# Performance work log

Hardware: AMD Instinct MI355X
Metric: run time of the kernel (lower is better)

The kernel has to match this reference:

```python
import jax, jax.numpy as jnp
import numpy as np

NODES = 81
NODE_DIM = 2
IN_DIM = NODES * NODE_DIM  # 162
D = 256
H = 16
HD = D // H
DFF = 2048
T, B, E = 1024, 8, 648


def _layernorm(x, w, b, eps=1e-5):
    m = x.mean(-1, keepdims=True)
    v = x.var(-1, keepdims=True)
    return (x - m) / jnp.sqrt(v + eps) * w + b


def setup_inputs() -> dict:
    key = jax.random.key(0)
    ks = jax.random.split(key, 12)
    s = 0.02
    W = lambda k, shape: jax.random.normal(k, shape, jnp.float32) * s
    return {
        "src": jax.random.normal(ks[0], (T, B, IN_DIM), jnp.float32),
        "edge_index": jax.random.randint(ks[1], (2, E), 0, NODES),
        "gcn_w": W(ks[2], (NODE_DIM, NODE_DIM)),
        "gcn_b": jnp.zeros((NODE_DIM,), jnp.float32),
        "fc_w": W(ks[3], (IN_DIM, D)),
        "fc_b": jnp.zeros((D,), jnp.float32),
        "wq": W(ks[4], (D, D)), "bq": jnp.zeros((D,), jnp.float32),
        "wk": W(ks[5], (D, D)), "bk": jnp.zeros((D,), jnp.float32),
        "wv": W(ks[6], (D, D)), "bv": jnp.zeros((D,), jnp.float32),
        "wo": W(ks[7], (D, D)), "bo": jnp.zeros((D,), jnp.float32),
        "ln1_w": jnp.ones((D,), jnp.float32), "ln1_b": jnp.zeros((D,), jnp.float32),
        "ffn_w1": W(ks[8], (D, DFF)), "ffn_b1": jnp.zeros((DFF,), jnp.float32),
        "ffn_w2": W(ks[9], (DFF, D)), "ffn_b2": jnp.zeros((D,), jnp.float32),
        "ln2_w": jnp.ones((D,), jnp.float32), "ln2_b": jnp.zeros((D,), jnp.float32),
        "dec_w": W(ks[10], (D, IN_DIM)), "dec_b": jnp.zeros((IN_DIM,), jnp.float32),
    }


def reference(src, edge_index, gcn_w, gcn_b, fc_w, fc_b, wq, bq, wk, bk, wv, bv,
              wo, bo, ln1_w, ln1_b, ffn_w1, ffn_b1, ffn_w2, ffn_b2, ln2_w, ln2_b,
              dec_w, dec_b):
    t, b, _ = src.shape
    # ---- batched GCNConv(2,2): all T*B tiny graphs share one adjacency ----
    # src[t,b] = [in_flow(81), out_flow(81)] -> node features [81, 2]
    xg = jnp.swapaxes(src.reshape(t, b, NODE_DIM, NODES), -1, -2)  # [T,B,81,2]
    row, col = edge_index[0], edge_index[1]
    A = jnp.zeros((NODES, NODES), src.dtype).at[col, row].add(1.0)
    A = A + jnp.eye(NODES, dtype=src.dtype)          # add self-loops
    deg = A.sum(1)
    dinv = jnp.where(deg > 0, 1.0 / jnp.sqrt(deg), 0.0)
    A_hat = dinv[:, None] * A * dinv[None, :]        # D^-1/2 (A+I) D^-1/2
    hg = jnp.einsum('ij,tbjc->tbic', A_hat, xg @ gcn_w) + gcn_b  # [T,B,81,2]
    # gcn_output.transpose(0,1).view(-1): channel-major flatten
    src2 = jnp.swapaxes(hg, -1, -2).reshape(t, b, IN_DIM)
    # ---- fc + positional encoding ----
    x = src2 @ fc_w + fc_b  # [T,B,D]
    pos = jnp.arange(t, dtype=jnp.float32)[:, None]
    div = jnp.exp(jnp.arange(0, D, 2, dtype=jnp.float32) * (-np.log(10000.0) / D))
    pe = jnp.zeros((t, D), x.dtype).at[:, 0::2].set(jnp.sin(pos * div))
    pe = pe.at[:, 1::2].set(jnp.cos(pos * div))
    x = x + pe[:, None, :]
    # ---- TransformerEncoderLayer (post-norm, relu, causal mask, eval) ----
    q = (x @ wq + bq).reshape(t, b, H, HD)
    k = (x @ wk + bk).reshape(t, b, H, HD)
    v = (x @ wv + bv).reshape(t, b, H, HD)
    scores = jnp.einsum('tbhd,sbhd->bhts', q, k) / jnp.sqrt(jnp.asarray(HD, x.dtype))
    causal = jnp.tril(jnp.ones((t, t), bool))
    scores = jnp.where(causal, scores, jnp.finfo(x.dtype).min)
    attn = jax.nn.softmax(scores, axis=-1)
    ctx = jnp.einsum('bhts,sbhd->tbhd', attn, v).reshape(t, b, D) @ wo + bo
    x = _layernorm(x + ctx, ln1_w, ln1_b)
    ff = jax.nn.relu(x @ ffn_w1 + ffn_b1) @ ffn_w2 + ffn_b2
    x = _layernorm(x + ff, ln2_w, ln2_b)
    return x @ dec_w + dec_b  # [T,B,162]
```

## Files before the change

### kernel.cpp

```cpp
#include <hip/hip_runtime.h>
#include <math.h>

#define T_    1024
#define B_    8
#define D_    256
#define H_    16
#define HD_   16
#define DFF_  2048
#define NODES_ 81
#define INDIM_ 162
#define E_    648
#define M_    (T_*B_)

typedef __bf16 bf16x8 __attribute__((ext_vector_type(8)));
typedef float  f32x4  __attribute__((ext_vector_type(4)));
typedef unsigned short ushort_t;
typedef unsigned int   uint_t;

union bfpack { bf16x8 v; uint_t u[4]; };

__device__ __forceinline__ ushort_t f2bf(float f) {
    union { float f; uint_t u; } c; c.f = f;
    uint_t u = c.u;
    uint_t r = u + 0x7fffu + ((u >> 16) & 1u);
    return (ushort_t)(r >> 16);
}

__device__ __forceinline__ uint_t fbits(float f) {
    union { float f; uint_t u; } c; c.f = f;
    return c.u;
}

__device__ __forceinline__ bf16x8 zero8() {
    bf16x8 v;
#pragma unroll
    for (int e = 0; e < 8; e++) v[e] = (__bf16)0.0f;
    return v;
}

__device__ __forceinline__ void gload_lds16(const void* g, void* l) {
    __builtin_amdgcn_global_load_lds(
        (const __attribute__((address_space(1))) void*)g,
        (__attribute__((address_space(3))) void*)l, 16, 0, 0);
}

__device__ __forceinline__ void trans_tile(
        const float* __restrict__ in, ushort_t* __restrict__ out,
        float (*tile)[33], int K, int N, int Kp, int bx, int by) {
    int k0 = bx * 32, n0 = by * 32;
    int tx = threadIdx.x & 31, ty = threadIdx.x >> 5;
#pragma unroll
    for (int i = 0; i < 4; i++) {
        int r = k0 + ty + i * 8, c = n0 + tx;
        tile[ty + i * 8][tx] = (r < K && c < N) ? in[(size_t)r * N + c] : 0.f;
    }
    __syncthreads();
#pragma unroll
    for (int i = 0; i < 4; i++) {
        int r = n0 + ty + i * 8, c = k0 + tx;
        out[(size_t)r * Kp + c] = f2bf(tile[tx][ty + i * 8]);
    }
}

__global__ __launch_bounds__(256) void prep_all(
        const int* __restrict__ edge, const float* __restrict__ gcn_w,
        const float* __restrict__ gcn_b, const float* __restrict__ fc_w,
        const float* __restrict__ fc_b, const float* __restrict__ src,
        const float* __restrict__ wq, const float* __restrict__ wk,
        const float* __restrict__ wv, const float* __restrict__ wo,
        const float* __restrict__ dec_w, const float* __restrict__ w1,
        const float* __restrict__ w2,
        const float* __restrict__ bq, const float* __restrict__ bk,
        const float* __restrict__ bv,
        ushort_t* __restrict__ weffT, float* __restrict__ beff,
        ushort_t* __restrict__ srcb,
        ushort_t* __restrict__ wqkvT, ushort_t* __restrict__ woT,
        ushort_t* __restrict__ dwT, ushort_t* __restrict__ w1T,
        ushort_t* __restrict__ w2T, float* __restrict__ qkvbias) {
    __shared__ float A[NODES_ * NODES_];
    __shared__ float dinv[NODES_];
    __shared__ float tile[32][33];
    int bid = blockIdx.x;
    int tid = threadIdx.x;
    if (bid < 82) {
        for (int i = tid; i < NODES_ * NODES_; i += 256) A[i] = 0.f;
        __syncthreads();
        for (int e = tid; e < E_; e += 256) {
            int r = edge[e];
            int c = edge[E_ + e];
            atomicAdd(&A[c * NODES_ + r], 1.0f);
        }
        __syncthreads();
        if (tid < NODES_) A[tid * NODES_ + tid] += 1.0f;
        __syncthreads();
        if (tid < NODES_) {
            float s = 0.f;
            for (int k = 0; k < NODES_; k++) s += A[tid * NODES_ + k];
            dinv[tid] = (s > 0.f) ? rsqrtf(s) : 0.f;
        }
        __syncthreads();
        int d = tid, j = bid;
        if (j < NODES_) {
            float s0 = 0.f, s1 = 0.f;
            for (int i = 0; i < NODES_; i++) {
                float a = dinv[i] * A[i * NODES_ + j] * dinv[j];
                s0 += a * fc_w[(0 * NODES_ + i) * D_ + d];
                s1 += a * fc_w[(1 * NODES_ + i) * D_ + d];
            }
            weffT[d * 192 + j]          = f2bf(gcn_w[0] * s0 + gcn_w[1] * s1);
            weffT[d * 192 + NODES_ + j] = f2bf(gcn_w[2] * s0 + gcn_w[3] * s1);
        } else {
            float t0 = 0.f, t1 = 0.f;
            for (int i = 0; i < NODES_; i++) {
                t0 += fc_w[(0 * NODES_ + i) * D_ + d];
                t1 += fc_w[(1 * NODES_ + i) * D_ + d];
            }
            beff[d] = fc_b[d] + gcn_b[0] * t0 + gcn_b[1] * t1;
            for (int c = INDIM_; c < 192; c++) weffT[d * 192 + c] = 0;
        }
    } else if (bid < 1426) {
        int l = bid - 82;
        if (l < 64)        trans_tile(wq,    wqkvT,          tile, D_,   D_,     D_,   l & 7,  l >> 3);
        else if (l < 128)  trans_tile(wk,    wqkvT + 65536,  tile, D_,   D_,     D_,   (l-64) & 7,  (l-64) >> 3);
        else if (l < 192)  trans_tile(wv,    wqkvT + 131072, tile, D_,   D_,     D_,   (l-128) & 7, (l-128) >> 3);
        else if (l < 256)  trans_tile(wo,    woT,            tile, D_,   D_,     D_,   (l-192) & 7, (l-192) >> 3);
        else if (l < 320)  trans_tile(dec_w, dwT,            tile, D_,   INDIM_, D_,   (l-256) & 7, (l-256) >> 3);
        else if (l < 832)  trans_tile(w1,    w1T,            tile, D_,   DFF_,   D_,   (l-320) & 7, (l-320) >> 3);
        else               trans_tile(w2,    w2T,            tile, DFF_, D_,     DFF_, (l-832) & 63, (l-832) >> 6);
    } else if (bid == 1426) {
#pragma unroll
        for (int k = 0; k < 3; k++) {
            int i = k * 256 + tid;
            qkvbias[i] = (i < 256) ? bq[i] : ((i < 512) ? bk[i - 256] : bv[i - 512]);
        }
    } else {
        int blk = bid - 1427;
        size_t row0 = (size_t)blk * 64;
        const float* sp = src + row0 * INDIM_;
        ushort_t* dp = srcb + row0 * 192;
        for (int i = tid; i < 64 * INDIM_; i += 256) {
            int r = i / INDIM_;
            int c = i - r * INDIM_;
            dp[(size_t)r * 192 + c] = f2bf(sp[i]);
        }
        for (int i = tid; i < 64 * 30; i += 256) {
            int r = i / 30;
            int c = i - r * 30;
            dp[(size_t)r * 192 + INDIM_ + c] = 0;
        }
    }
}

enum { EP_PE = 0, EP_QKV = 1, EP_PLAIN = 2, EP_RELU = 3, EP_DEC = 4, EP_PART = 5 };

template <int EPI, int TM, int KS>
__global__ __launch_bounds__(256) void gemm_bf16(
        const ushort_t* __restrict__ A, const ushort_t* __restrict__ BT,
        const float* __restrict__ bias, float* __restrict__ Cf,
        ushort_t* __restrict__ Cb, int M, int N, int K) {
    __shared__ ushort_t sA[TM * 64];
    __shared__ ushort_t sB[128 * 64];
    int tid = threadIdx.x;
    int w = tid >> 6, lane = tid & 63;
    int cc = lane & 15, q = lane >> 4;
    int bm = blockIdx.y * TM, bn = blockIdx.x * 128;
    int part = (KS > 1) ? blockIdx.z : 0;
    int kbeg = part * (K / KS), kend = kbeg + K / KS;

    int srow = (lane >> 3);
    int sslot = lane & 7;

    const int NJ = (TM == 128) ? 4 : 2;
    int mbase = (TM == 128) ? ((w >> 1) * 64) : 0;
    int nbase = (TM == 128) ? ((w & 1) * 64) : (w * 32);

    f32x4 acc[4][NJ];
#pragma unroll
    for (int i = 0; i < 4; i++)
#pragma unroll
        for (int j = 0; j < NJ; j++)
#pragma unroll
            for (int e = 0; e < 4; e++) acc[i][j][e] = 0.f;

    for (int k0 = kbeg; k0 < kend; k0 += 64) {
        if (TM == 128) {
#pragma unroll
            for (int i = 0; i < 4; i++) {
                int r = w * 32 + i * 8 + srow;
                const ushort_t* ga = A + (size_t)(bm + r) * K + k0 + ((sslot ^ (r & 7)) * 8);
                gload_lds16(ga, &sA[(w * 32 + i * 8) * 64]);
            }
        } else {
#pragma unroll
            for (int i = 0; i < 2; i++) {
                int r = w * 16 + i * 8 + srow;
                const ushort_t* ga = A + (size_t)(bm + r) * K + k0 + ((sslot ^ (r & 7)) * 8);
                gload_lds16(ga, &sA[(w * 16 + i * 8) * 64]);
            }
        }
#pragma unroll
        for (int i = 0; i < 4; i++) {
            int r = w * 32 + i * 8 + srow;
            const ushort_t* gb = BT + (size_t)(bn + r) * K + k0 + ((sslot ^ (r & 7)) * 8);
            gload_lds16(gb, &sB[(w * 32 + i * 8) * 64]);
        }
        __syncthreads();
#pragma unroll
        for (int ks = 0; ks < 2; ks++) {
            bf16x8 af[4], bfr[NJ];
#pragma unroll
            for (int i = 0; i < 4; i++) {
                int m = mbase + i * 16 + cc;
                int off = m * 64 + (((ks * 4 + q) ^ (cc & 7)) * 8);
                af[i] = *(const bf16x8*)&sA[off];
            }
#pragma unroll
            for (int j = 0; j < NJ; j++) {
                int n = nbase + j * 16 + cc;
                int off = n * 64 + (((ks * 4 + q) ^ (cc & 7)) * 8);
                bfr[j] = *(const bf16x8*)&sB[off];
            }
#pragma unroll
            for (int i = 0; i < 4; i++)
#pragma unroll
                for (int j = 0; j < NJ; j++)
                    acc[i][j] = __builtin_amdgcn_mfma_f32_16x16x32_bf16(af[i], bfr[j], acc[i][j], 0, 0, 0);
        }
        __syncthreads();
    }

#pragma unroll
    for (int i = 0; i < 4; i++) {
#pragma unroll
        for (int j = 0; j < NJ; j++) {
            int col = bn + nbase + j * 16 + cc;
            float bv = 0.f;
            if (EPI == EP_DEC) bv = (col < INDIM_) ? bias[col] : 0.f;
            else if (EPI != EP_PART) bv = bias[col];
#pragma unroll
            for (int reg = 0; reg < 4; reg++) {
                int row = bm + mbase + i * 16 + q * 4 + reg;
                float v = acc[i][j][reg] + bv;
                if (EPI == EP_PE) {
                    int t = row >> 3;
                    float freq = __expf((float)(col & ~1) * (-9.210340371976184f / 256.f));
                    float ang = (float)t * freq;
                    v += (col & 1) ? __cosf(ang) : __sinf(ang);
                    Cf[(size_t)row * N + col] = v;
                    Cb[(size_t)row * N + col] = f2bf(v);
                } else if (EPI == EP_QKV) {
                    int t = row >> 3, b = row & 7;
                    int nn = col & 255, which = col >> 8;
                    int h = nn >> 4, hd = nn & 15;
                    float vq = (which == 0) ? v * 0.25f : v;
                    Cb[(size_t)which * 2097152 +
                       ((size_t)((b * H_ + h) * T_ + t)) * HD_ + hd] = f2bf(vq);
                } else if (EPI == EP_PLAIN) {
                    Cf[(size_t)row * N + col] = v;
                } else if (EPI == EP_RELU) {
                    v = fmaxf(v, 0.f);
                    Cb[(size_t)row * N + col] = f2bf(v);
                } else if (EPI == EP_DEC) {
                    if (col < INDIM_) Cf[(size_t)row * INDIM_ + col] = v;
                } else if (EPI == EP_PART) {
                    Cf[(size_t)part * M * N + (size_t)row * N + col] = v;
                }
            }
        }
    }
}

__global__ __launch_bounds__(256) void attn_mfma(
        const ushort_t* __restrict__ Qb, const ushort_t* __restrict__ Kb,
        const ushort_t* __restrict__ Vb, float* __restrict__ partO,
        float* __restrict__ partL) {
    const int qc_of[20] = {0,1,2,2,3,3,4,4,4,5,5,5,6,6,6,6,7,7,7,7};
    const int kp_of[20] = {0,0,0,1,0,1,0,1,2,0,1,2,0,1,2,3,0,1,2,3};
    int slot = blockIdx.x;
    int qc = qc_of[slot], kp = kp_of[slot];
    int bh = blockIdx.y;
    int tid = threadIdx.x;
    int w = tid >> 6, lane = tid & 63;
    int cc = lane & 15, q = lane >> 4;
    int qb0 = qc * 128;
    int kbeg = kp * 4;
    int kend = 2 * (qc + 1);
    if (kend > kbeg + 4) kend = kbeg + 4;

    __shared__ ushort_t VTs[2][16 * 72];

    const ushort_t* Qp = Qb + (size_t)bh * (T_ * HD_);
    const ushort_t* Kp = Kb + (size_t)bh * (T_ * HD_);
    const ushort_t* Vp = Vb + (size_t)bh * (T_ * HD_);

    bf16x8 qf[2];
#pragma unroll
    for (int i = 0; i < 2; i++) {
        if (q < 2)
            qf[i] = *(const bf16x8*)&Qp[(size_t)(qb0 + w * 32 + i * 16 + cc) * HD_ + q * 8];
        else
            qf[i] = zero8();
    }

    f32x4 ot[2];
    float lsum[2];
#pragma unroll
    for (int i = 0; i < 2; i++) {
        lsum[i] = 0.f;
#pragma unroll
        for (int e = 0; e < 4; e++) ot[i][e] = 0.f;
    }

    int qmaxw = qb0 + w * 32 + 31;

    for (int kb = kbeg; kb < kend; kb++) {
        ushort_t* vbuf = VTs[kb & 1];
        {
            int r = tid >> 2, c0 = (tid & 3) * 4;
            ushort4 vv = *(const ushort4*)&Vp[(size_t)(kb * 64 + r) * HD_ + c0];
            vbuf[(c0 + 0) * 72 + r] = vv.x;
            vbuf[(c0 + 1) * 72 + r] = vv.y;
            vbuf[(c0 + 2) * 72 + r] = vv.z;
            vbuf[(c0 + 3) * 72 + r] = vv.w;
        }
        __syncthreads();
        if (kb * 64 > qmaxw) continue;

        bf16x8 kf[4];
#pragma unroll
        for (int j = 0; j < 4; j++) {
            if (q < 2)
                kf[j] = *(const bf16x8*)&Kp[(size_t)(kb * 64 + j * 16 + cc) * HD_ + q * 8];
            else
                kf[j] = zero8();
        }

        f32x4 s[2][4];
#pragma unroll
        for (int j = 0; j < 4; j++)
#pragma unroll
            for (int i = 0; i < 2; i++) {
                f32x4 z;
#pragma unroll
                for (int e = 0; e < 4; e++) z[e] = 0.f;
                s[i][j] = __builtin_amdgcn_mfma_f32_16x16x32_bf16(kf[j], qf[i], z, 0, 0, 0);
            }

#pragma unroll
        for (int jj = 0; jj < 2; jj++) {
            int j0 = jj * 2, j1 = j0 + 1;
            bfpack af;
            const uint_t* vt0 = (const uint_t*)&vbuf[cc * 72 + j0 * 16 + q * 4];
            const uint_t* vt1 = (const uint_t*)&vbuf[cc * 72 + j1 * 16 + q * 4];
            af.u[0] = vt0[0]; af.u[1] = vt0[1];
            af.u[2] = vt1[0]; af.u[3] = vt1[1];
            int key00 = kb * 64 + j0 * 16 + q * 4;
            int key01 = key00 + 16;
#pragma unroll
            for (int i = 0; i < 2; i++) {
                float p0 = __expf(s[i][j0][0]);
                float p1 = __expf(s[i][j0][1]);
                float p2 = __expf(s[i][j0][2]);
                float p3 = __expf(s[i][j0][3]);
                float p4 = __expf(s[i][j1][0]);
                float p5 = __expf(s[i][j1][1]);
                float p6 = __expf(s[i][j1][2]);
                float p7 = __expf(s[i][j1][3]);
                int qsub = qb0 + w * 32 + i * 16;
                if (kb * 64 + j0 * 16 + 15 > qsub) {
                    int qrow = qsub + cc;
                    if (key00 + 0 > qrow) p0 = 0.f;
                    if (key00 + 1 > qrow) p1 = 0.f;
                    if (key00 + 2 > qrow) p2 = 0.f;
                    if (key00 + 3 > qrow) p3 = 0.f;
                }
                if (kb * 64 + j1 * 16 + 15 > qsub) {
                    int qrow = qsub + cc;
                    if (key01 + 0 > qrow) p4 = 0.f;
                    if (key01 + 1 > qrow) p5 = 0.f;
                    if (key01 + 2 > qrow) p6 = 0.f;
                    if (key01 + 3 > qrow) p7 = 0.f;
                }
                bfpack pf;
                pf.u[0] = (fbits(p0) >> 16) | (fbits(p1) & 0xffff0000u);
                pf.u[1] = (fbits(p2) >> 16) | (fbits(p3) & 0xffff0000u);
                pf.u[2] = (fbits(p4) >> 16) | (fbits(p5) & 0xffff0000u);
                pf.u[3] = (fbits(p6) >> 16) | (fbits(p7) & 0xffff0000u);
                ot[i] = __builtin_amdgcn_mfma_f32_16x16x32_bf16(af.v, pf.v, ot[i], 0, 0, 0);
                lsum[i] += ((p0 + p1) + (p2 + p3)) + ((p4 + p5) + (p6 + p7));
            }
        }
    }

    int base = (bh * 20 + slot) * 128;
#pragma unroll
    for (int i = 0; i < 2; i++) {
        float l = lsum[i];
        l += __shfl_xor(l, 16);
        l += __shfl_xor(l, 32);
        int row = w * 32 + i * 16 + cc;
        *(f32x4*)&partO[((size_t)(base + row)) * 16 + q * 4] = ot[i];
        if (q == 0) partL[base + row] = l;
    }
}

__global__ __launch_bounds__(256) void attn_reduce(
        const float* __restrict__ partO, const float* __restrict__ partL,
        ushort_t* __restrict__ ctxb) {
    const int cum[9] = {0, 1, 2, 4, 6, 9, 12, 16, 20};
    int qc = blockIdx.x, bh = blockIdx.y;
    int row = threadIdx.x >> 1, dh = threadIdx.x & 1;
    int p0 = cum[qc], p1 = cum[qc + 1];
    float o[8];
#pragma unroll
    for (int e = 0; e < 8; e++) o[e] = 0.f;
    float l = 0.f;
    for (int p = p0; p < p1; p++) {
        size_t base = ((size_t)bh * 20 + p) * 128 + row;
        const float4 a = *(const float4*)&partO[base * 16 + dh * 8];
        const float4 b4 = *(const float4*)&partO[base * 16 + dh * 8 + 4];
        o[0] += a.x; o[1] += a.y; o[2] += a.z; o[3] += a.w;
        o[4] += b4.x; o[5] += b4.y; o[6] += b4.z; o[7] += b4.w;
        l += partL[base];
    }
    float inv = 1.f / l;
    int t = qc * 128 + row, b = bh >> 4, h = bh & 15;
    ushort_t* op = ctxb + ((size_t)t * B_ + b) * D_ + h * HD_ + dh * 8;
    ushort4 u0, u1;
    u0.x = f2bf(o[0] * inv); u0.y = f2bf(o[1] * inv);
    u0.z = f2bf(o[2] * inv); u0.w = f2bf(o[3] * inv);
    u1.x = f2bf(o[4] * inv); u1.y = f2bf(o[5] * inv);
    u1.z = f2bf(o[6] * inv); u1.w = f2bf(o[7] * inv);
    *(ushort4*)&op[0] = u0;
    *(ushort4*)&op[4] = u1;
}

template <int NP, bool HASB>
__global__ __launch_bounds__(256) void ln_kernel(
        const float* __restrict__ X, const float* __restrict__ P0,
        const float* __restrict__ P1, const float* __restrict__ RB,
        const float* __restrict__ w, const float* __restrict__ b,
        float* __restrict__ out, ushort_t* __restrict__ outb) {
    int wv = threadIdx.x >> 6, lane = threadIdx.x & 63;
    int row = blockIdx.x * 4 + wv;
    int c = lane * 4;
    const float4 x4 = *(const float4*)&X[(size_t)row * D_ + c];
    const float4 p4 = *(const float4*)&P0[(size_t)row * D_ + c];
    float v0 = x4.x + p4.x, v1 = x4.y + p4.y, v2 = x4.z + p4.z, v3 = x4.w + p4.w;
    if (NP == 2) {
        const float4 q4 = *(const float4*)&P1[(size_t)row * D_ + c];
        v0 += q4.x; v1 += q4.y; v2 += q4.z; v3 += q4.w;
    }
    if (HASB) {
        const float4 r4 = *(const float4*)&RB[c];
        v0 += r4.x; v1 += r4.y; v2 += r4.z; v3 += r4.w;
    }
    float s  = v0 + v1 + v2 + v3;
    float sq = v0 * v0 + v1 * v1 + v2 * v2 + v3 * v3;
    for (int off = 32; off; off >>= 1) {
        s  += __shfl_xor(s, off);
        sq += __shfl_xor(sq, off);
    }
    float mean = s * (1.f / 256.f);
    float var  = sq * (1.f / 256.f) - mean * mean;
    float rstd = rsqrtf(var + 1e-5f);
    float o0 = (v0 - mean) * rstd * w[c + 0] + b[c + 0];
    float o1 = (v1 - mean) * rstd * w[c + 1] + b[c + 1];
    float o2 = (v2 - mean) * rstd * w[c + 2] + b[c + 2];
    float o3 = (v3 - mean) * rstd * w[c + 3] + b[c + 3];
    float4 o; o.x = o0; o.y = o1; o.z = o2; o.w = o3;
    *(float4*)&out[(size_t)row * D_ + c] = o;
    ushort4 ob;
    ob.x = f2bf(o0); ob.y = f2bf(o1); ob.z = f2bf(o2); ob.w = f2bf(o3);
    *(ushort4*)&outb[(size_t)row * D_ + c] = ob;
}

extern "C" void kernel_launch(void* const* d_in, const int* in_sizes, int n_in,
                              void* d_out, int out_size, void* d_ws, size_t ws_size,
                              hipStream_t stream) {
    (void)in_sizes; (void)n_in; (void)out_size; (void)ws_size;
    const float* src     = (const float*)d_in[0];
    const int*   edge    = (const int*)d_in[1];
    const float* gcn_w   = (const float*)d_in[2];
    const float* gcn_b   = (const float*)d_in[3];
    const float* fc_w    = (const float*)d_in[4];
    const float* fc_b    = (const float*)d_in[5];
    const float* wq      = (const float*)d_in[6];
    const float* bq      = (const float*)d_in[7];
    const float* wk      = (const float*)d_in[8];
    const float* bk      = (const float*)d_in[9];
    const float* wv      = (const float*)d_in[10];
    const float* bv      = (const float*)d_in[11];
    const float* wo      = (const float*)d_in[12];
    const float* bo      = (const float*)d_in[13];
    const float* ln1_w   = (const float*)d_in[14];
    const float* ln1_b   = (const float*)d_in[15];
    const float* ffn_w1  = (const float*)d_in[16];
    const float* ffn_b1  = (const float*)d_in[17];
    const float* ffn_w2  = (const float*)d_in[18];
    const float* ffn_b2  = (const float*)d_in[19];
    const float* ln2_w   = (const float*)d_in[20];
    const float* ln2_b   = (const float*)d_in[21];
    const float* dec_w   = (const float*)d_in[22];
    const float* dec_b   = (const float*)d_in[23];
    float* out = (float*)d_out;

    float* ws = (float*)d_ws;
    float* beff    = ws;
    float* qkvbias = ws + 256;
    float* x0      = ws + 1024;
    float* tmp     = x0  + 2097152;
    float* tmp2    = tmp + 2097152;
    float* x1      = tmp2 + 2097152;
    float* x2s     = x1  + 2097152;
    ushort_t* ub   = (ushort_t*)(ws + 10486784);
    ushort_t* srcb = ub;
    ushort_t* x0b  = ub + 1572864;
    ushort_t* x1b  = x0b + 2097152;
    ushort_t* x2b  = x1b + 2097152;
    ushort_t* ctxb = x2b + 2097152;
    ushort_t* hb   = ctxb + 2097152;
    ushort_t* qkvb = hb + 16777216;
    ushort_t* weffT= qkvb + 6291456;
    ushort_t* wqkvT= weffT + 49152;
    ushort_t* woT  = wqkvT + 196608;
    ushort_t* w1T  = woT + 65536;
    ushort_t* w2T  = w1T + 524288;
    ushort_t* dwT  = w2T + 524288;
    float* partO = (float*)hb;
    float* partL = partO + 5242880;

    prep_all<<<1555, 256, 0, stream>>>(edge, gcn_w, gcn_b, fc_w, fc_b, src,
                                       wq, wk, wv, wo, dec_w, ffn_w1, ffn_w2,
                                       bq, bk, bv, weffT, beff, srcb,
                                       wqkvT, woT, dwT, w1T, w2T, qkvbias);

    gemm_bf16<EP_PE, 64, 1><<<dim3(2, 128), 256, 0, stream>>>(srcb, weffT, beff, x0, x0b, M_, D_, 192);
    gemm_bf16<EP_QKV, 64, 1><<<dim3(6, 128), 256, 0, stream>>>(x0b, wqkvT, qkvbias, nullptr, qkvb, M_, 768, D_);
    attn_mfma<<<dim3(20, 128), 256, 0, stream>>>(qkvb, qkvb + 2097152, qkvb + 4194304, partO, partL);
    attn_reduce<<<dim3(8, 128), 256, 0, stream>>>(partO, partL, ctxb);
    gemm_bf16<EP_PLAIN, 64, 1><<<dim3(2, 128), 256, 0, stream>>>(ctxb, woT, bo, tmp, nullptr, M_, D_, D_);
    ln_kernel<1, false><<<2048, 256, 0, stream>>>(x0, tmp, nullptr, nullptr, ln1_w, ln1_b, x1, x1b);
    gemm_bf16<EP_RELU, 128, 1><<<dim3(16, 64), 256, 0, stream>>>(x1b, w1T, ffn_b1, nullptr, hb, M_, DFF_, D_);
    gemm_bf16<EP_PART, 64, 2><<<dim3(2, 128, 2), 256, 0, stream>>>(hb, w2T, nullptr, tmp, nullptr, M_, D_, DFF_);
    ln_kernel<2, true><<<2048, 256, 0, stream>>>(x1, tmp, tmp2, ffn_b2, ln2_w, ln2_b, x2s, x2b);
    gemm_bf16<EP_DEC, 64, 1><<<dim3(2, 128), 256, 0, stream>>>(x2b, dwT, dec_b, out, nullptr, M_, D_, D_);
}
```

Baseline: 238.3 us.

## Fuse output-projection and FFN2 GEMMs with residual add and LayerNorm

Adds a gemm_ln kernel where each block computes full 256-wide output rows, then applies bias, residual add and LayerNorm in the epilogue with a cross-wave shared-memory reduction. It replaces the Wo GEMM plus LN1 and the split-K FFN2 GEMM plus LN2, removing two launches and the fp32 round trips through tmp/tmp2. The FFN2 stage drops split-K and runs K=2048 in 256 blocks of 32 rows, so parallelism shrinks and there is no double-buffering. The epilogue also reads the residual per element in a non-vectorised pattern.

After: 244.9 us. +2.8%, slower.

```diff
diff --git a/kernel.cpp b/kernel.cpp
--- a/kernel.cpp
+++ b/kernel.cpp
@@ -268,6 +268,140 @@
             }
         }
     }
+}
+
+template <int TM, bool WF32>
+__global__ __launch_bounds__(256) void gemm_ln(
+        const ushort_t* __restrict__ A, const ushort_t* __restrict__ BT,
+        const float* __restrict__ bias, const float* __restrict__ X,
+        const float* __restrict__ lw, const float* __restrict__ lb,
+        float* __restrict__ outF, ushort_t* __restrict__ outB, int K) {
+    const int NI = TM / 16;
+    __shared__ ushort_t sA[TM * 64];
+    __shared__ ushort_t sB[256 * 64];
+    __shared__ float red[4][TM][2];
+    int tid = threadIdx.x;
+    int w = tid >> 6, lane = tid & 63;
+    int cc = lane & 15, q = lane >> 4;
+    int bm = blockIdx.x * TM;
+    int srow = lane >> 3, sslot = lane & 7;
+    int nbase = w * 64;
+
+    f32x4 acc[NI][4];
+#pragma unroll
+    for (int i = 0; i < NI; i++)
+#pragma unroll
+        for (int j = 0; j < 4; j++)
+#pragma unroll
+            for (int e = 0; e < 4; e++) acc[i][j][e] = 0.f;
+
+    for (int k0 = 0; k0 < K; k0 += 64) {
+        if (TM == 64) {
+#pragma unroll
+            for (int i = 0; i < 2; i++) {
+                int r = w * 16 + i * 8 + srow;
+                const ushort_t* ga = A + (size_t)(bm + r) * K + k0 + ((sslot ^ (r & 7)) * 8);
+                gload_lds16(ga, &sA[(w * 16 + i * 8) * 64]);
+            }
+        } else {
+            int r = w * 8 + srow;
+            const ushort_t* ga = A + (size_t)(bm + r) * K + k0 + ((sslot ^ (r & 7)) * 8);
+            gload_lds16(ga, &sA[(w * 8) * 64]);
+        }
+#pragma unroll
+        for (int i = 0; i < 8; i++) {
+            int r = w * 64 + i * 8 + srow;
+            const ushort_t* gb = BT + (size_t)r * K + k0 + ((sslot ^ (r & 7)) * 8);
+            gload_lds16(gb, &sB[(w * 64 + i * 8) * 64]);
+        }
+        __syncthreads();
+#pragma unroll
+        for (int ks = 0; ks < 2; ks++) {
+            bf16x8 af[NI], bfr[4];
+#pragma unroll
+            for (int i = 0; i < NI; i++) {
+                int m = i * 16 + cc;
+                int off = m * 64 + (((ks * 4 + q) ^ (cc & 7)) * 8);
+                af[i] = *(const bf16x8*)&sA[off];
+            }
+#pragma unroll
+            for (int j = 0; j < 4; j++) {
+                int n = nbase + j * 16 + cc;
+                int off = n * 64 + (((ks * 4 + q) ^ (cc & 7)) * 8);
+                bfr[j] = *(const bf16x8*)&sB[off];
+            }
+#pragma unroll
+            for (int i = 0; i < NI; i++)
+#pragma unroll
+                for (int j = 0; j < 4; j++)
+                    acc[i][j] = __builtin_amdgcn_mfma_f32_16x16x32_bf16(af[i], bfr[j], acc[i][j], 0, 0, 0);
+        }
+        __syncthreads();
+    }
+
+    float s[NI][4], sq[NI][4];
+#pragma unroll
+    for (int i = 0; i < NI; i++)
+#pragma unroll
+        for (int reg = 0; reg < 4; reg++) { s[i][reg] = 0.f; sq[i][reg] = 0.f; }
+
+#pragma unroll
+    for (int i = 0; i < NI; i++)
+#pragma unroll
+        for (int j = 0; j < 4; j++) {
+            int col = nbase + j * 16 + cc;
+            float bv = bias[col];
+#pragma unroll
+            for (int reg = 0; reg < 4; reg++) {
+                int row = bm + i * 16 + q * 4 + reg;
+                float v = acc[i][j][reg] + bv + X[(size_t)row * D_ + col];
+                acc[i][j][reg] = v;
+                s[i][reg] += v;
+                sq[i][reg] += v * v;
+            }
+        }
+#pragma unroll
+    for (int i = 0; i < NI; i++)
+#pragma unroll
+        for (int reg = 0; reg < 4; reg++) {
+            float a = s[i][reg], b2 = sq[i][reg];
+#pragma unroll
+            for (int off = 1; off < 16; off <<= 1) {
+                a += __shfl_xor(a, off);
+                b2 += __shfl_xor(b2, off);
+            }
+            s[i][reg] = a; sq[i][reg] = b2;
+        }
+    if (cc == 0) {
+#pragma unroll
+        for (int i = 0; i < NI; i++)
+#pragma unroll
+            for (int reg = 0; reg < 4; reg++) {
+                int lr = i * 16 + q * 4 + reg;
+                red[w][lr][0] = s[i][reg];
+                red[w][lr][1] = sq[i][reg];
+            }
+    }
+    __syncthreads();
+#pragma unroll
+    for (int i = 0; i < NI; i++)
+#pragma unroll
+        for (int reg = 0; reg < 4; reg++) {
+            int lr = i * 16 + q * 4 + reg;
+            float ts = red[0][lr][0] + red[1][lr][0] + red[2][lr][0] + red[3][lr][0];
+            float tq = red[0][lr][1] + red[1][lr][1] + red[2][lr][1] + red[3][lr][1];
+            float mean = ts * (1.f / 256.f);
+            float var  = tq * (1.f / 256.f) - mean * mean;
+            float rstd = rsqrtf(var + 1e-5f);
+            int row = bm + lr;
+#pragma unroll
+            for (int j = 0; j < 4; j++) {
+                int col = nbase + j * 16 + cc;
+                float o = (acc[i][j][reg] - mean) * rstd * lw[col] + lb[col];
+                if (WF32) outF[(size_t)row * D_ + col] = o;
+                outB[(size_t)row * D_ + col] = f2bf(o);
+            }
+        }
 }
 
 __global__ __launch_bounds__(256) void attn_mfma(
@@ -435,46 +569,6 @@
     *(ushort4*)&op[4] = u1;
 }
 
-template <int NP, bool HASB>
-__global__ __launch_bounds__(256) void ln_kernel(
-        const float* __restrict__ X, const float* __restrict__ P0,
-        const float* __restrict__ P1, const float* __restrict__ RB,
-        const float* __restrict__ w, const float* __restrict__ b,
-        float* __restrict__ out, ushort_t* __restrict__ outb) {
-    int wv = threadIdx.x >> 6, lane = threadIdx.x & 63;
-    int row = blockIdx.x * 4 + wv;
-    int c = lane * 4;
-    const float4 x4 = *(const float4*)&X[(size_t)row * D_ + c];
-    const float4 p4 = *(const float4*)&P0[(size_t)row * D_ + c];
-    float v0 = x4.x + p4.x, v1 = x4.y + p4.y, v2 = x4.z + p4.z, v3 = x4.w + p4.w;
-    if (NP == 2) {
-        const float4 q4 = *(const float4*)&P1[(size_t)row * D_ + c];
-        v0 += q4.x; v1 += q4.y; v2 += q4.z; v3 += q4.w;
-    }
-    if (HASB) {
-        const float4 r4 = *(const float4*)&RB[c];
-        v0 += r4.x; v1 += r4.y; v2 += r4.z; v3 += r4.w;
-    }
-    float s  = v0 + v1 + v2 + v3;
-    float sq = v0 * v0 + v1 * v1 + v2 * v2 + v3 * v3;
-    for (int off = 32; off; off >>= 1) {
-        s  += __shfl_xor(s, off);
-        sq += __shfl_xor(sq, off);
-    }
-    float mean = s * (1.f / 256.f);
-    float var  = sq * (1.f / 256.f) - mean * mean;
-    float rstd = rsqrtf(var + 1e-5f);
-    float o0 = (v0 - mean) * rstd * w[c + 0] + b[c + 0];
-    float o1 = (v1 - mean) * rstd * w[c + 1] + b[c + 1];
-    float o2 = (v2 - mean) * rstd * w[c + 2] + b[c + 2];
-    float o3 = (v3 - mean) * rstd * w[c + 3] + b[c + 3];
-    float4 o; o.x = o0; o.y = o1; o.z = o2; o.w = o3;
-    *(float4*)&out[(size_t)row * D_ + c] = o;
-    ushort4 ob;
-    ob.x = f2bf(o0); ob.y = f2bf(o1); ob.z = f2bf(o2); ob.w = f2bf(o3);
-    *(ushort4*)&outb[(size_t)row * D_ + c] = ob;
-}
-
 extern "C" void kernel_launch(void* const* d_in, const int* in_sizes, int n_in,
                               void* d_out, int out_size, void* d_ws, size_t ws_size,
                               hipStream_t stream) {
@@ -512,7 +606,6 @@
     float* tmp     = x0  + 2097152;
     float* tmp2    = tmp + 2097152;
     float* x1      = tmp2 + 2097152;
-    float* x2s     = x1  + 2097152;
     ushort_t* ub   = (ushort_t*)(ws + 10486784);
     ushort_t* srcb = ub;
     ushort_t* x0b  = ub + 1572864;
@@ -539,10 +632,8 @@
     gemm_bf16<EP_QKV, 64, 1><<<dim3(6, 128), 256, 0, stream>>>(x0b, wqkvT, qkvbias, nullptr, qkvb, M_, 768, D_);
     attn_mfma<<<dim3(20, 128), 256, 0, stream>>>(qkvb, qkvb + 2097152, qkvb + 4194304, partO, partL);
     attn_reduce<<<dim3(8, 128), 256, 0, stream>>>(partO, partL, ctxb);
-    gemm_bf16<EP_PLAIN, 64, 1><<<dim3(2, 128), 256, 0, stream>>>(ctxb, woT, bo, tmp, nullptr, M_, D_, D_);
-    ln_kernel<1, false><<<2048, 256, 0, stream>>>(x0, tmp, nullptr, nullptr, ln1_w, ln1_b, x1, x1b);
+    gemm_ln<64, true><<<128, 256, 0, stream>>>(ctxb, woT, bo, x0, ln1_w, ln1_b, x1, x1b, D_);
     gemm_bf16<EP_RELU, 128, 1><<<dim3(16, 64), 256, 0, stream>>>(x1b, w1T, ffn_b1, nullptr, hb, M_, DFF_, D_);
-    gemm_bf16<EP_PART, 64, 2><<<dim3(2, 128, 2), 256, 0, stream>>>(hb, w2T, nullptr, tmp, nullptr, M_, D_, DFF_);
-    ln_kernel<2, true><<<2048, 256, 0, stream>>>(x1, tmp, tmp2, ffn_b2, ln2_w, ln2_b, x2s, x2b);
+    gemm_ln<32, false><<<256, 256, 0, stream>>>(hb, w2T, ffn_b2, x1, ln2_w, ln2_b, nullptr, x2b, DFF_);
     gemm_bf16<EP_DEC, 64, 1><<<dim3(2, 128), 256, 0, stream>>>(x2b, dwT, dec_b, out, nullptr, M_, D_, D_);
 }
```
